# Kernel tuning notes

Measured on AMD Instinct MI355X. Metric: run time of the kernel, lower is better.

The kernel has to match this reference:

```python
import math
import jax, jax.numpy as jnp
import numpy as np

_GELU_C = math.sqrt(2.0 / math.pi)

def _gelu_tanh(x):
    return 0.5 * x * (1.0 + jnp.tanh(_GELU_C * (x + 0.044715 * x * x * x)))

def _l2_normalize(v, eps=1e-12):
    # matches F.normalize: v / max(||v||, eps)
    n = jnp.sqrt(jnp.sum(v * v, axis=-1, keepdims=True))
    return v / jnp.maximum(n, eps)

def setup_inputs() -> dict:
    key = jax.random.key(0)
    k1, k2, k3 = jax.random.split(key, 3)
    B, T, D = 8, 2048, 1024
    x = jax.random.normal(k1, (B, T, D), dtype=jnp.float32)
    # nn.Parameter initial values from the module
    log_alpha = jnp.asarray(math.log(math.exp(0.5) - 1.0), dtype=jnp.float32)
    log_sigma = jnp.asarray(math.log(1.0), dtype=jnp.float32)
    return {"x": x, "log_alpha": log_alpha, "log_sigma": log_sigma}

def reference(x, log_alpha, log_sigma):
    B, T, D = x.shape
    alpha = jax.nn.softplus(log_alpha)
    sigma = jax.nn.softplus(log_sigma)
    scale = 1.0 / math.sqrt(D)
    # full strictly-past causal attention (triu with diagonal=0 masks self too)
    sim = jnp.einsum('btd,bsd->bts', x, x) * scale            # [B,T,T]
    causal = jnp.triu(jnp.ones((T, T), dtype=bool), k=0)      # True = masked
    sim = jnp.where(causal[None], -jnp.inf, sim)
    # NaN-safe masked softmax: fully-masked rows (t=0) -> all zeros,
    # matching torch softmax + nan_to_num(nan=0.0)
    m = jnp.max(sim, axis=-1, keepdims=True)
    m_safe = jnp.where(jnp.isfinite(m), m, 0.0)
    e = jnp.exp(sim - m_safe)                                 # -inf -> 0
    denom = jnp.sum(e, axis=-1, keepdims=True)
    attn = jnp.where(denom > 0, e / jnp.where(denom > 0, denom, 1.0), 0.0)
    context = jnp.einsum('bts,bsd->btd', attn, x)             # [B,T,D]
    cos_sim = jnp.sum(_l2_normalize(x) * _l2_normalize(context), axis=-1)  # [B,T]
    novelty = jnp.clip(1.0 - cos_sim, 0.0, 2.0) / 2.0
    novelty = jnp.nan_to_num(novelty, nan=1.0)
    gate = 1.0 + alpha * jnp.tanh(sigma * novelty[..., None])
    return _gelu_tanh(x * gate)
```

## Files before the change

### kernel.cpp

```cpp
#include <hip/hip_runtime.h>
#include <math.h>

#define TN 2048
#define DN 1024
#define NEG_INF (-3.0e38f)

typedef __attribute__((ext_vector_type(8))) _Float16 half8;
typedef __attribute__((ext_vector_type(4))) _Float16 half4v;
typedef __attribute__((ext_vector_type(2))) _Float16 half2v;
typedef __attribute__((ext_vector_type(4))) float f32x4;

__device__ __forceinline__ f32x4 mfma16(half8 a, half8 b, f32x4 c) {
  return __builtin_amdgcn_mfma_f32_16x16x32_f16(a, b, c, 0, 0, 0);
}

#define BAR_LDS()  asm volatile("s_waitcnt lgkmcnt(0)\ns_barrier" ::: "memory")
#define BAR_ALL()  asm volatile("s_waitcnt vmcnt(0) lgkmcnt(0)\ns_barrier" ::: "memory")

__device__ __forceinline__ int img_off(int key, int f) {
  const int kg = key >> 2;
  const int p  = ((kg & 1) << 2) | (kg >> 1);
  return (f >> 4) * 512 + p * 64 + (key & 3) * 16 + (f & 15);
}

__global__ __launch_bounds__(256) void convert_x(const float* __restrict__ x,
                                                 _Float16* __restrict__ w) {
  const long long gid = (long long)blockIdx.x * 256 + threadIdx.x;
  const long long e   = gid * 8;
  const int bt   = (int)(e >> 15);
  const int et   = (int)(e & 32767);
  const int f16b = et >> 9;
  const int p    = (et >> 6) & 7;
  const int row  = (et >> 4) & 3;
  const int col0 = et & 15;
  const int kg   = ((p & 3) << 1) | (p >> 2);
  const int key  = kg * 4 + row;
  const size_t xoff = ((size_t)bt * 32 + key) * DN + f16b * 16 + col0;
  float4 u0 = *(const float4*)(x + xoff);
  float4 u1 = *(const float4*)(x + xoff + 4);
  half8 h = {(_Float16)u0.x, (_Float16)u0.y, (_Float16)u0.z, (_Float16)u0.w,
             (_Float16)u1.x, (_Float16)u1.y, (_Float16)u1.z, (_Float16)u1.w};
  *(half8*)(w + e) = h;
}

#define ISSUE4(T, O0, O1, O2, O3)                                             \
  asm volatile("ds_read_b64_tr_b16 %0, %4 offset:" O0 "\n\t"                  \
               "ds_read_b64_tr_b16 %1, %4 offset:" O1 "\n\t"                  \
               "ds_read_b64_tr_b16 %2, %4 offset:" O2 "\n\t"                  \
               "ds_read_b64_tr_b16 %3, %4 offset:" O3                         \
               : "=&v"(T[0]), "=&v"(T[1]), "=&v"(T[2]), "=&v"(T[3])           \
               : "v"(ab));

#define MFMA4(T, CT0, CT1)                                                    \
  {                                                                           \
    half8 bf0 = __builtin_shufflevector(T[0], T[1], 0, 1, 2, 3, 4, 5, 6, 7);  \
    half8 bf1 = __builtin_shufflevector(T[2], T[3], 0, 1, 2, 3, 4, 5, 6, 7);  \
    oacc[0][CT0] = mfma16(a0, bf0, oacc[0][CT0]);                             \
    oacc[1][CT0] = mfma16(a1, bf0, oacc[1][CT0]);                             \
    oacc[0][CT1] = mfma16(a0, bf1, oacc[0][CT1]);                             \
    oacc[1][CT1] = mfma16(a1, bf1, oacc[1][CT1]);                             \
  }

template <bool WS>
__global__ __launch_bounds__(512)
void attn_gate(const float* __restrict__ x, const _Float16* __restrict__ wsx,
               const float* __restrict__ pla, const float* __restrict__ pls,
               float* __restrict__ out) {
  __shared__ _Float16 Kbuf[2][32768];
  __shared__ _Float16 SredH[8][32][17][2];
  __shared__ _Float16 Pq[32][40];
  __shared__ float m_s[32], l_s[32], corr_s[32], gate_s[32];
  __shared__ int resc_s;

  const int tid = threadIdx.x;
  const int w   = tid >> 6;
  const int l   = tid & 63;
  const int lr  = l & 15;
  const int lg  = l >> 4;
  const int kq  = w;

  const int b  = blockIdx.x & 7;
  const int pr = blockIdx.x >> 3;

  const float alpha = log1pf(expf(pla[0]));
  const float sigma = log1pf(expf(pls[0]));

  const float* xb = x + (size_t)b * TN * DN;
  float*       ob = out + (size_t)b * TN * DN;

  const int kg0 = lr >> 2;
  const int bk0 = ((((kg0 & 1) << 2) | (kg0 >> 1)) << 6) + (lr & 3) * 16 + (lg & 1) * 8;
  const int kg1 = 4 + (lr >> 2);
  const int bk1 = ((((kg1 & 1) << 2) | (kg1 >> 1)) << 6) + (lr & 3) * 16 + (lg & 1) * 8;

  for (int hv = 0; hv < 2; ++hv) {
    const int qt    = hv ? (63 - pr) : pr;
    const int qbase = qt * 32;
    const int nkt   = qt + 1;

    if constexpr (WS) {
      const _Float16* t0 = wsx + (size_t)(b * 64 + 0) * 32768;
#pragma unroll
      for (int i = 0; i < 8; ++i)
        __builtin_amdgcn_global_load_lds(
            (const __attribute__((address_space(1))) void*)(t0 + w * 4096 + i * 512 + l * 8),
            (__attribute__((address_space(3))) void*)(&Kbuf[0][w * 4096 + i * 512]), 16, 0, 0);
      if (nkt > 1) {
        const _Float16* t1 = wsx + (size_t)(b * 64 + 1) * 32768;
#pragma unroll
        for (int i = 0; i < 8; ++i)
          __builtin_amdgcn_global_load_lds(
              (const __attribute__((address_space(1))) void*)(t1 + w * 4096 + i * 512 + l * 8),
              (__attribute__((address_space(3))) void*)(&Kbuf[1][w * 4096 + i * 512]), 16, 0, 0);
      }
    } else {
      const int skey = tid >> 4, sc = tid & 15;
      for (int t = 0; t < (nkt > 1 ? 2 : 1); ++t) {
        const float* kp = xb + (size_t)(t * 32 + skey) * DN + sc * 4;
#pragma unroll
        for (int j = 0; j < 16; ++j) {
          const int f = sc * 4 + 64 * j;
          float4 v = *(const float4*)(kp + 64 * j);
          half4v h = {(_Float16)v.x, (_Float16)v.y, (_Float16)v.z, (_Float16)v.w};
          *(half4v*)&Kbuf[t][img_off(skey, f)] = h;
        }
      }
    }

    half8 qf0[4], qf1[4];
    if constexpr (WS) {
      const _Float16* qtile = wsx + (size_t)(b * 64 + qt) * 32768;
      const int r0  = lr;
      const int g0  = r0 >> 2;
      const int qp0 = (((g0 & 1) << 2) | (g0 >> 1)) * 64 + (r0 & 3) * 16 + (lg & 1) * 8;
      const int r1  = 16 + lr;
      const int g1  = r1 >> 2;
      const int qp1 = (((g1 & 1) << 2) | (g1 >> 1)) * 64 + (r1 & 3) * 16 + (lg & 1) * 8;
#pragma unroll
      for (int s = 0; s < 4; ++s) {
        const int base = (kq * 8 + s * 2 + (lg >> 1)) * 512;
        qf0[s] = *(const half8*)&qtile[base + qp0];
        qf1[s] = *(const half8*)&qtile[base + qp1];
      }
    } else {
#pragma unroll
      for (int s = 0; s < 4; ++s) {
        const float* qp0 = xb + (size_t)(qbase + lr) * DN + kq * 128 + s * 32 + lg * 8;
        const float* qp1 = xb + (size_t)(qbase + 16 + lr) * DN + kq * 128 + s * 32 + lg * 8;
        float4 a = ((const float4*)qp0)[0];
        float4 c = ((const float4*)qp0)[1];
        half8 h0;
        h0[0]=(_Float16)a.x; h0[1]=(_Float16)a.y; h0[2]=(_Float16)a.z; h0[3]=(_Float16)a.w;
        h0[4]=(_Float16)c.x; h0[5]=(_Float16)c.y; h0[6]=(_Float16)c.z; h0[7]=(_Float16)c.w;
        qf0[s] = h0;
        a = ((const float4*)qp1)[0];
        c = ((const float4*)qp1)[1];
        half8 h1;
        h1[0]=(_Float16)a.x; h1[1]=(_Float16)a.y; h1[2]=(_Float16)a.z; h1[3]=(_Float16)a.w;
        h1[4]=(_Float16)c.x; h1[5]=(_Float16)c.y; h1[6]=(_Float16)c.z; h1[7]=(_Float16)c.w;
        qf1[s] = h1;
      }
    }

    f32x4 oacc[2][8];
#pragma unroll
    for (int rt = 0; rt < 2; ++rt)
#pragma unroll
      for (int ct = 0; ct < 8; ++ct)
        oacc[rt][ct] = f32x4{0.f, 0.f, 0.f, 0.f};

    if (tid < 32) { m_s[tid] = NEG_INF; l_s[tid] = 0.0f; }
    if (tid == 0) resc_s = 0;
    BAR_ALL();

    for (int kt = 0; kt < nkt; ++kt) {
      const int cur = kt & 1;

      {
        f32x4 s00 = f32x4{0.f,0.f,0.f,0.f}, s01 = f32x4{0.f,0.f,0.f,0.f};
        f32x4 s10 = f32x4{0.f,0.f,0.f,0.f}, s11 = f32x4{0.f,0.f,0.f,0.f};
        const _Float16* kb = &Kbuf[cur][0];
#pragma unroll
        for (int s = 0; s < 4; ++s) {
          const int base = (kq * 8 + s * 2 + (lg >> 1)) * 512;
          half8 bf0 = *(const half8*)&kb[base + bk0];
          half8 bf1 = *(const half8*)&kb[base + bk1];
          s00 = mfma16(qf0[s], bf0, s00);
          s10 = mfma16(qf1[s], bf0, s10);
          s01 = mfma16(qf0[s], bf1, s01);
          s11 = mfma16(qf1[s], bf1, s11);
        }
#pragma unroll
        for (int j = 0; j < 4; ++j) {
          half2v p0 = {(_Float16)s00[j], (_Float16)s01[j]};
          *(half2v*)&SredH[kq][lg * 4 + j][lr][0] = p0;
          half2v p1 = {(_Float16)s10[j], (_Float16)s11[j]};
          *(half2v*)&SredH[kq][16 + lg * 4 + j][lr][0] = p1;
        }
      }
      BAR_LDS();

      {
        const int r   = tid >> 4;
        const int c0  = tid & 15;
        const int qg  = qbase + r;
        const int kb0 = kt * 32;
        float s0 = 0.f, s1 = 0.f;
#pragma unroll
        for (int k8 = 0; k8 < 8; ++k8) {
          half2v v = *(const half2v*)&SredH[k8][r][c0][0];
          s0 += (float)v[0];
          s1 += (float)v[1];
        }
        s0 *= 0.03125f; s1 *= 0.03125f;
        const bool v0 = (kb0 + c0)      < qg;
        const bool v1 = (kb0 + c0 + 16) < qg;
        if (!v0) s0 = NEG_INF;
        if (!v1) s1 = NEG_INF;
        float tmax = fmaxf(s0, s1);
#pragma unroll
        for (int d = 1; d < 16; d <<= 1) tmax = fmaxf(tmax, __shfl_xor(tmax, d));
        const float m_old = m_s[r];
        const float m_new = fmaxf(m_old, tmax);
        float p0 = v0 ? __expf(s0 - m_new) : 0.0f;
        float p1 = v1 ? __expf(s1 - m_new) : 0.0f;
        float ps = p0 + p1;
#pragma unroll
        for (int d = 1; d < 16; d <<= 1) ps += __shfl_xor(ps, d);
        if (c0 == 0) {
          const float corr = (m_old > 0.5f * NEG_INF) ? __expf(m_old - m_new) : 0.0f;
          m_s[r]    = m_new;
          l_s[r]    = l_s[r] * corr + ps;
          corr_s[r] = corr;
          if (m_new > m_old) resc_s = 1;
        }
        Pq[r][c0]      = (_Float16)p0;
        Pq[r][c0 + 16] = (_Float16)p1;
      }
      BAR_LDS();

      {
        const int doresc = resc_s;
        if (doresc) {
#pragma unroll
          for (int rt = 0; rt < 2; ++rt)
#pragma unroll
            for (int j = 0; j < 4; ++j) {
              const float cr2 = corr_s[rt * 16 + lg * 4 + j];
#pragma unroll
              for (int ct = 0; ct < 8; ++ct) oacc[rt][ct][j] *= cr2;
            }
        }
        const uint32_t pa0 = (uint32_t)(uintptr_t)(void*)&Pq[lr][lg * 8];
        const uint32_t pa1 = (uint32_t)(uintptr_t)(void*)&Pq[16 + lr][lg * 8];
        const uint32_t ab  = (uint32_t)(uintptr_t)(void*)&Kbuf[cur][w * 4096 + l * 4];
        asm volatile("s_waitcnt lgkmcnt(0)" ::: "memory");
        __builtin_amdgcn_sched_barrier(0);
        half8 a0, a1;
        half4v t0[4], t1[4];
        asm volatile("ds_read_b128 %0, %2\n\t"
                     "ds_read_b128 %1, %3"
                     : "=&v"(a0), "=&v"(a1) : "v"(pa0), "v"(pa1));
        ISSUE4(t0, "0", "512", "1024", "1536");
        ISSUE4(t1, "2048", "2560", "3072", "3584");
        asm volatile("s_waitcnt lgkmcnt(4)" ::: "memory");
        __builtin_amdgcn_sched_barrier(0);
        MFMA4(t0, 0, 1);
        ISSUE4(t0, "4096", "4608", "5120", "5632");
        asm volatile("s_waitcnt lgkmcnt(4)" ::: "memory");
        __builtin_amdgcn_sched_barrier(0);
        MFMA4(t1, 2, 3);
        ISSUE4(t1, "6144", "6656", "7168", "7680");
        asm volatile("s_waitcnt lgkmcnt(4)" ::: "memory");
        __builtin_amdgcn_sched_barrier(0);
        MFMA4(t0, 4, 5);
        asm volatile("s_waitcnt lgkmcnt(0)" ::: "memory");
        __builtin_amdgcn_sched_barrier(0);
        MFMA4(t1, 6, 7);
      }
      BAR_ALL();

      if (kt + 2 < nkt) {
        if constexpr (WS) {
          const _Float16* tn = wsx + (size_t)(b * 64 + kt + 2) * 32768;
#pragma unroll
          for (int i = 0; i < 8; ++i)
            __builtin_amdgcn_global_load_lds(
                (const __attribute__((address_space(1))) void*)(tn + w * 4096 + i * 512 + l * 8),
                (__attribute__((address_space(3))) void*)(&Kbuf[cur][w * 4096 + i * 512]), 16, 0, 0);
        } else {
          const int skey = tid >> 4, sc = tid & 15;
          const float* kp = xb + (size_t)((kt + 2) * 32 + skey) * DN + sc * 4;
#pragma unroll
          for (int j = 0; j < 16; ++j) {
            const int f = sc * 4 + 64 * j;
            float4 v = *(const float4*)(kp + 64 * j);
            half4v h = {(_Float16)v.x, (_Float16)v.y, (_Float16)v.z, (_Float16)v.w};
            *(half4v*)&Kbuf[cur][img_off(skey, f)] = h;
          }
        }
      }
    }

    {
      float* ered = (float*)&SredH[0][0][0][0];
#pragma unroll
      for (int rt = 0; rt < 2; ++rt)
#pragma unroll
        for (int j = 0; j < 4; ++j) {
          const int row = rt * 16 + lg * 4 + j;
          const float* xr = xb + (size_t)(qbase + row) * DN + w * 128 + lr;
          float a1 = 0.f, a2 = 0.f, a3 = 0.f;
#pragma unroll
          for (int ct = 0; ct < 8; ++ct) {
            const float xv = xr[ct * 16];
            const float ov = oacc[rt][ct][j];
            a1 += xv * ov; a2 += xv * xv; a3 += ov * ov;
          }
#pragma unroll
          for (int d = 1; d < 16; d <<= 1) {
            a1 += __shfl_xor(a1, d);
            a2 += __shfl_xor(a2, d);
            a3 += __shfl_xor(a3, d);
          }
          if (lr == 0) {
            float* e = ered + (row * 8 + w) * 4;
            e[0] = a1; e[1] = a2; e[2] = a3;
          }
        }
    }
    __syncthreads();
    if (tid < 32) {
      const float* ered = (const float*)&SredH[0][0][0][0];
      float SxO = 0.f, Sxx = 0.f, SOO = 0.f;
#pragma unroll
      for (int wv = 0; wv < 8; ++wv) {
        const float* e = ered + (tid * 8 + wv) * 4;
        SxO += e[0]; Sxx += e[1]; SOO += e[2];
      }
      const float lden = l_s[tid];
      float cosv = 0.0f;
      if (lden > 0.0f) {
        const float nx = fmaxf(sqrtf(Sxx), 1e-12f);
        const float nc = fmaxf(sqrtf(SOO) / lden, 1e-12f);
        cosv = (SxO / lden) / (nx * nc);
      }
      float nov = fminf(fmaxf(1.0f - cosv, 0.0f), 2.0f) * 0.5f;
      gate_s[tid] = 1.0f + alpha * tanhf(sigma * nov);
    }
    __syncthreads();
    {
#pragma unroll
      for (int rt = 0; rt < 2; ++rt)
#pragma unroll
        for (int j = 0; j < 4; ++j) {
          const int row = rt * 16 + lg * 4 + j;
          const float g = gate_s[row];
          const float* xr = xb + (size_t)(qbase + row) * DN + w * 128 + lr;
          float* orow     = ob + (size_t)(qbase + row) * DN + w * 128 + lr;
#pragma unroll
          for (int ct = 0; ct < 8; ++ct) {
            const float z = xr[ct * 16] * g;
            const float u = 0.7978845608028654f * (z + 0.044715f * z * z * z);
            orow[ct * 16] = 0.5f * z * (1.0f + tanhf(u));
          }
        }
    }
    __syncthreads();
  }
}

extern "C" void kernel_launch(void* const* d_in, const int* in_sizes, int n_in,
                              void* d_out, int out_size, void* d_ws, size_t ws_size,
                              hipStream_t stream) {
  const float* x  = (const float*)d_in[0];
  const float* la = (const float*)d_in[1];
  const float* ls = (const float*)d_in[2];
  float* out = (float*)d_out;
  const size_t need = (size_t)8 * 64 * 32768 * 2;
  if (ws_size >= need) {
    convert_x<<<dim3(8192), dim3(256), 0, stream>>>(x, (_Float16*)d_ws);
    attn_gate<true><<<dim3(256), dim3(512), 0, stream>>>(
        x, (const _Float16*)d_ws, la, ls, out);
  } else {
    attn_gate<false><<<dim3(256), dim3(512), 0, stream>>>(
        x, (const _Float16*)nullptr, la, ls, out);
  }
}
```

Measured before the change: 203.7 us.

## Software-pipeline QK of next tile with PV of current tile in flash loop

Restructures the per-tile loop so the QK^T MFMAs for tile t+1 are issued alongside the PV MFMAs for tile t, and the softmax for t+1 runs after staging the next K tile. This cuts the per-iteration barrier count from three to two and aims to overlap matrix work from the two stages. It also replaces the block-wide rescale flag with a per-row check on the correction factor, removing a shared-memory flag. The cost is higher register pressure from keeping S accumulators live during PV, plus a more intricate ordering of the shared buffers (SredH and Pq) across the two barriers.

```diff
diff --git a/kernel.cpp b/kernel.cpp
--- a/kernel.cpp
+++ b/kernel.cpp
@@ -70,7 +70,6 @@
   __shared__ _Float16 SredH[8][32][17][2];
   __shared__ _Float16 Pq[32][40];
   __shared__ float m_s[32], l_s[32], corr_s[32], gate_s[32];
-  __shared__ int resc_s;
 
   const int tid = threadIdx.x;
   const int w   = tid >> 6;
@@ -98,34 +97,29 @@
     const int qbase = qt * 32;
     const int nkt   = qt + 1;
 
-    if constexpr (WS) {
-      const _Float16* t0 = wsx + (size_t)(b * 64 + 0) * 32768;
-#pragma unroll
-      for (int i = 0; i < 8; ++i)
-        __builtin_amdgcn_global_load_lds(
-            (const __attribute__((address_space(1))) void*)(t0 + w * 4096 + i * 512 + l * 8),
-            (__attribute__((address_space(3))) void*)(&Kbuf[0][w * 4096 + i * 512]), 16, 0, 0);
-      if (nkt > 1) {
-        const _Float16* t1 = wsx + (size_t)(b * 64 + 1) * 32768;
+    auto STAGE = [&](int t) {
+      if constexpr (WS) {
+        const _Float16* tn = wsx + (size_t)(b * 64 + t) * 32768;
 #pragma unroll
         for (int i = 0; i < 8; ++i)
           __builtin_amdgcn_global_load_lds(
-              (const __attribute__((address_space(1))) void*)(t1 + w * 4096 + i * 512 + l * 8),
-              (__attribute__((address_space(3))) void*)(&Kbuf[1][w * 4096 + i * 512]), 16, 0, 0);
-      }
-    } else {
-      const int skey = tid >> 4, sc = tid & 15;
-      for (int t = 0; t < (nkt > 1 ? 2 : 1); ++t) {
+              (const __attribute__((address_space(1))) void*)(tn + w * 4096 + i * 512 + l * 8),
+              (__attribute__((address_space(3))) void*)(&Kbuf[t & 1][w * 4096 + i * 512]), 16, 0, 0);
+      } else {
+        const int skey = tid >> 4, sc = tid & 15;
         const float* kp = xb + (size_t)(t * 32 + skey) * DN + sc * 4;
 #pragma unroll
         for (int j = 0; j < 16; ++j) {
           const int f = sc * 4 + 64 * j;
           float4 v = *(const float4*)(kp + 64 * j);
           half4v h = {(_Float16)v.x, (_Float16)v.y, (_Float16)v.z, (_Float16)v.w};
-          *(half4v*)&Kbuf[t][img_off(skey, f)] = h;
+          *(half4v*)&Kbuf[t & 1][img_off(skey, f)] = h;
         }
       }
-    }
+    };
+
+    STAGE(0);
+    if (nkt > 1) STAGE(1);
 
     half8 qf0[4], qf1[4];
     if constexpr (WS) {
@@ -170,90 +164,90 @@
         oacc[rt][ct] = f32x4{0.f, 0.f, 0.f, 0.f};
 
     if (tid < 32) { m_s[tid] = NEG_INF; l_s[tid] = 0.0f; }
-    if (tid == 0) resc_s = 0;
     BAR_ALL();
 
-    for (int kt = 0; kt < nkt; ++kt) {
-      const int cur = kt & 1;
-
+    auto QK = [&](int t) {
+      f32x4 s00 = f32x4{0.f,0.f,0.f,0.f}, s01 = f32x4{0.f,0.f,0.f,0.f};
+      f32x4 s10 = f32x4{0.f,0.f,0.f,0.f}, s11 = f32x4{0.f,0.f,0.f,0.f};
+      const _Float16* kb = &Kbuf[t & 1][0];
+#pragma unroll
+      for (int s = 0; s < 4; ++s) {
+        const int base = (kq * 8 + s * 2 + (lg >> 1)) * 512;
+        half8 bf0 = *(const half8*)&kb[base + bk0];
+        half8 bf1 = *(const half8*)&kb[base + bk1];
+        s00 = mfma16(qf0[s], bf0, s00);
+        s10 = mfma16(qf1[s], bf0, s10);
+        s01 = mfma16(qf0[s], bf1, s01);
+        s11 = mfma16(qf1[s], bf1, s11);
+      }
+#pragma unroll
+      for (int j = 0; j < 4; ++j) {
+        half2v p0 = {(_Float16)s00[j], (_Float16)s01[j]};
+        *(half2v*)&SredH[kq][lg * 4 + j][lr][0] = p0;
+        half2v p1 = {(_Float16)s10[j], (_Float16)s11[j]};
+        *(half2v*)&SredH[kq][16 + lg * 4 + j][lr][0] = p1;
+      }
+    };
+
+    auto SM = [&](int t) {
+      const int r   = tid >> 4;
+      const int c0  = tid & 15;
+      const int qg  = qbase + r;
+      const int kb0 = t * 32;
+      float s0 = 0.f, s1 = 0.f;
+#pragma unroll
+      for (int k8 = 0; k8 < 8; ++k8) {
+        half2v v = *(const half2v*)&SredH[k8][r][c0][0];
+        s0 += (float)v[0];
+        s1 += (float)v[1];
+      }
+      s0 *= 0.03125f; s1 *= 0.03125f;
+      const bool v0 = (kb0 + c0)      < qg;
+      const bool v1 = (kb0 + c0 + 16) < qg;
+      if (!v0) s0 = NEG_INF;
+      if (!v1) s1 = NEG_INF;
+      float tmax = fmaxf(s0, s1);
+#pragma unroll
+      for (int d = 1; d < 16; d <<= 1) tmax = fmaxf(tmax, __shfl_xor(tmax, d));
+      const float m_old = m_s[r];
+      const float m_new = fmaxf(m_old, tmax);
+      float p0 = v0 ? __expf(s0 - m_new) : 0.0f;
+      float p1 = v1 ? __expf(s1 - m_new) : 0.0f;
+      float ps = p0 + p1;
+#pragma unroll
+      for (int d = 1; d < 16; d <<= 1) ps += __shfl_xor(ps, d);
+      if (c0 == 0) {
+        const float corr = (m_old > 0.5f * NEG_INF) ? __expf(m_old - m_new) : 0.0f;
+        m_s[r]    = m_new;
+        l_s[r]    = l_s[r] * corr + ps;
+        corr_s[r] = corr;
+      }
+      Pq[r][c0]      = (_Float16)p0;
+      Pq[r][c0 + 16] = (_Float16)p1;
+    };
+
+    QK(0);
+    BAR_LDS();
+    SM(0);
+    BAR_LDS();
+
+    for (int t = 0; t < nkt; ++t) {
       {
-        f32x4 s00 = f32x4{0.f,0.f,0.f,0.f}, s01 = f32x4{0.f,0.f,0.f,0.f};
-        f32x4 s10 = f32x4{0.f,0.f,0.f,0.f}, s11 = f32x4{0.f,0.f,0.f,0.f};
-        const _Float16* kb = &Kbuf[cur][0];
-#pragma unroll
-        for (int s = 0; s < 4; ++s) {
-          const int base = (kq * 8 + s * 2 + (lg >> 1)) * 512;
-          half8 bf0 = *(const half8*)&kb[base + bk0];
-          half8 bf1 = *(const half8*)&kb[base + bk1];
-          s00 = mfma16(qf0[s], bf0, s00);
-          s10 = mfma16(qf1[s], bf0, s10);
-          s01 = mfma16(qf0[s], bf1, s01);
-          s11 = mfma16(qf1[s], bf1, s11);
-        }
-#pragma unroll
-        for (int j = 0; j < 4; ++j) {
-          half2v p0 = {(_Float16)s00[j], (_Float16)s01[j]};
-          *(half2v*)&SredH[kq][lg * 4 + j][lr][0] = p0;
-          half2v p1 = {(_Float16)s10[j], (_Float16)s11[j]};
-          *(half2v*)&SredH[kq][16 + lg * 4 + j][lr][0] = p1;
-        }
-      }
-      BAR_LDS();
-
-      {
-        const int r   = tid >> 4;
-        const int c0  = tid & 15;
-        const int qg  = qbase + r;
-        const int kb0 = kt * 32;
-        float s0 = 0.f, s1 = 0.f;
-#pragma unroll
-        for (int k8 = 0; k8 < 8; ++k8) {
-          half2v v = *(const half2v*)&SredH[k8][r][c0][0];
-          s0 += (float)v[0];
-          s1 += (float)v[1];
-        }
-        s0 *= 0.03125f; s1 *= 0.03125f;
-        const bool v0 = (kb0 + c0)      < qg;
-        const bool v1 = (kb0 + c0 + 16) < qg;
-        if (!v0) s0 = NEG_INF;
-        if (!v1) s1 = NEG_INF;
-        float tmax = fmaxf(s0, s1);
-#pragma unroll
-        for (int d = 1; d < 16; d <<= 1) tmax = fmaxf(tmax, __shfl_xor(tmax, d));
-        const float m_old = m_s[r];
-        const float m_new = fmaxf(m_old, tmax);
-        float p0 = v0 ? __expf(s0 - m_new) : 0.0f;
-        float p1 = v1 ? __expf(s1 - m_new) : 0.0f;
-        float ps = p0 + p1;
-#pragma unroll
-        for (int d = 1; d < 16; d <<= 1) ps += __shfl_xor(ps, d);
-        if (c0 == 0) {
-          const float corr = (m_old > 0.5f * NEG_INF) ? __expf(m_old - m_new) : 0.0f;
-          m_s[r]    = m_new;
-          l_s[r]    = l_s[r] * corr + ps;
-          corr_s[r] = corr;
-          if (m_new > m_old) resc_s = 1;
-        }
-        Pq[r][c0]      = (_Float16)p0;
-        Pq[r][c0 + 16] = (_Float16)p1;
-      }
-      BAR_LDS();
-
-      {
-        const int doresc = resc_s;
-        if (doresc) {
-#pragma unroll
-          for (int rt = 0; rt < 2; ++rt)
-#pragma unroll
-            for (int j = 0; j < 4; ++j) {
-              const float cr2 = corr_s[rt * 16 + lg * 4 + j];
+#pragma unroll
+        for (int rt = 0; rt < 2; ++rt)
+#pragma unroll
+          for (int j = 0; j < 4; ++j) {
+            const float cr2 = corr_s[rt * 16 + lg * 4 + j];
+            if (cr2 < 1.0f) {
 #pragma unroll
               for (int ct = 0; ct < 8; ++ct) oacc[rt][ct][j] *= cr2;
             }
-        }
+          }
+        if (t + 1 < nkt) QK(t + 1);
+
         const uint32_t pa0 = (uint32_t)(uintptr_t)(void*)&Pq[lr][lg * 8];
         const uint32_t pa1 = (uint32_t)(uintptr_t)(void*)&Pq[16 + lr][lg * 8];
-        const uint32_t ab  = (uint32_t)(uintptr_t)(void*)&Kbuf[cur][w * 4096 + l * 4];
+        const uint32_t ab  = (uint32_t)(uintptr_t)(void*)&Kbuf[t & 1][w * 4096 + l * 4];
         asm volatile("s_waitcnt lgkmcnt(0)" ::: "memory");
         __builtin_amdgcn_sched_barrier(0);
         half8 a0, a1;
@@ -278,28 +272,11 @@
         __builtin_amdgcn_sched_barrier(0);
         MFMA4(t1, 6, 7);
       }
+      BAR_LDS();
+
+      if (t + 2 < nkt) STAGE(t + 2);
+      if (t + 1 < nkt) SM(t + 1);
       BAR_ALL();
-
-      if (kt + 2 < nkt) {
-        if constexpr (WS) {
-          const _Float16* tn = wsx + (size_t)(b * 64 + kt + 2) * 32768;
-#pragma unroll
-          for (int i = 0; i < 8; ++i)
-            __builtin_amdgcn_global_load_lds(
-                (const __attribute__((address_space(1))) void*)(tn + w * 4096 + i * 512 + l * 8),
-                (__attribute__((address_space(3))) void*)(&Kbuf[cur][w * 4096 + i * 512]), 16, 0, 0);
-        } else {
-          const int skey = tid >> 4, sc = tid & 15;
-          const float* kp = xb + (size_t)((kt + 2) * 32 + skey) * DN + sc * 4;
-#pragma unroll
-          for (int j = 0; j < 16; ++j) {
-            const int f = sc * 4 + 64 * j;
-            float4 v = *(const float4*)(kp + 64 * j);
-            half4v h = {(_Float16)v.x, (_Float16)v.y, (_Float16)v.z, (_Float16)v.w};
-            *(half4v*)&Kbuf[cur][img_off(skey, f)] = h;
-          }
-        }
-      }
     }
 
     {
```

After: 219.0 us. +7.6%, slower.
